# Optimization experiments

Hardware: AMD Instinct MI355X
Metric: run time of the kernel (lower is better)

## Reference

```python
import jax, jax.numpy as jnp
import numpy as np


def _retain(o1, others, W, bias):
    # o1: (b, s, h); others: (b, 4, s, h); W: (h, h); bias: (1,)
    q = o1 @ W                                        # (b, s, h)
    scores = jnp.einsum('bih,bkjh->bijk', q, others) + bias[0]  # (b, s1, s2, 4)
    w = jax.nn.softmax(scores, axis=-1)               # softmax over the 4 options
    # weight[:, :, :, k] @ option_k summed over k
    return jnp.einsum('bijk,bkjh->bih', w, others)


def setup_inputs() -> dict:
    key = jax.random.key(0)
    ks = jax.random.split(key, 7)
    b, s, h = 32, 256, 1024
    opts = {f'option{i+1}': jax.random.normal(ks[i], (b, s, h), dtype=jnp.float32)
            for i in range(5)}
    W = 0.02 * jax.random.normal(ks[5], (h, h), dtype=jnp.float32)
    bias = 0.02 * jax.random.normal(ks[6], (1,), dtype=jnp.float32)
    return {**opts, 'W': W, 'bias': bias}


def reference(option1, option2, option3, option4, option5, W, bias):
    opts = [option1, option2, option3, option4, option5]
    total = None
    for i in range(5):
        others = jnp.stack([opts[j] for j in range(5) if j != i], axis=1)  # (b,4,s,h)
        r = _retain(opts[i], others, W, bias)
        total = r if total is None else total + r
    return total / 2.0
```

## Files before the change

### kernel.cpp

```cpp
#include <hip/hip_runtime.h>
#include <hip/hip_bf16.h>
#include <stdint.h>


#define BB 32
#define SS 256
#define HH 1024

typedef __attribute__((ext_vector_type(4))) float f32x4;
typedef __attribute__((ext_vector_type(8))) __bf16 bf16x8;
typedef __attribute__((ext_vector_type(4))) __bf16 bf16x4;

__device__ constexpr int PAIR(int i, int n) { return i * 4 + (n > i ? n - 1 : n); }

__global__ void canary(float* out, float v) { out[0] = v; }

__global__ __launch_bounds__(256) void cast_all(
    const float* p0, const float* p1, const float* p2, const float* p3, const float* p4,
    __bf16* __restrict__ dst)
{
  int m = blockIdx.x >> 12;
  long off = ((long)(blockIdx.x & 4095) * 256 + threadIdx.x) * 8;
  const float* src = m == 0 ? p0 : m == 1 ? p1 : m == 2 ? p2 : m == 3 ? p3 : p4;
  float4 v0 = *(const float4*)(src + off);
  float4 v1 = *(const float4*)(src + off + 4);
  bf16x8 h;
  h[0] = (__bf16)v0.x; h[1] = (__bf16)v0.y; h[2] = (__bf16)v0.z; h[3] = (__bf16)v0.w;
  h[4] = (__bf16)v1.x; h[5] = (__bf16)v1.y; h[6] = (__bf16)v1.z; h[7] = (__bf16)v1.w;
  *(bf16x8*)(dst + (long)m * BB * SS * HH + off) = h;
}

__global__ __launch_bounds__(256) void cast_trW(const float* __restrict__ src,
                                                __bf16* __restrict__ dstT)
{
  __shared__ __bf16 tile[64][72];
  int ct = blockIdx.x & 15, rt = blockIdx.x >> 4;
  const float* s = src + (long)(rt * 64) * 1024 + ct * 64;
  int t = threadIdx.x;
#pragma unroll
  for (int p = 0; p < 4; p++) {
    int c = t + p * 256;
    int row = c >> 4, c4 = c & 15;
    float4 v = *(const float4*)(s + (long)row * 1024 + c4 * 4);
    bf16x4 h;
    h[0] = (__bf16)v.x; h[1] = (__bf16)v.y; h[2] = (__bf16)v.z; h[3] = (__bf16)v.w;
    *(bf16x4*)&tile[row][c4 * 4] = h;
  }
  __syncthreads();
#pragma unroll
  for (int p = 0; p < 4; p++) {
    int c = t + p * 256;
    int hr = c >> 4, s4 = c & 15;
    bf16x4 h;
    h[0] = tile[s4 * 4 + 0][hr];
    h[1] = tile[s4 * 4 + 1][hr];
    h[2] = tile[s4 * 4 + 2][hr];
    h[3] = tile[s4 * 4 + 3][hr];
    *(bf16x4*)(dstT + (long)(ct * 64 + hr) * 1024 + rt * 64 + s4 * 4) = h;
  }
}

__global__ __launch_bounds__(512, 2) void qgemm256(
    const __bf16* __restrict__ A, const __bf16* __restrict__ Bt, __bf16* __restrict__ C)
{
  __shared__ __align__(16) char ldsb[2 * 65536];
  int lin = blockIdx.x;
  int xcd = lin & 7, idx = lin >> 3;
  int rt = xcd * 20 + (idx >> 2), ct = idx & 3;
  int t = threadIdx.x, l = t & 63, w = t >> 6;
  int wr = w >> 2, wc = w & 3;
  f32x4 acc[8][4] = {};

  const char* gp[8];
  int wdst[8];
#pragma unroll
  for (int p = 0; p < 8; p++) {
    int c = t + 512 * (p & 3);
    int row = c >> 3, slot = c & 7;
    int wb = row * 128 + ((slot ^ (row & 7)) << 4);
    if (p < 4) {
      gp[p] = (const char*)(A + (long)(rt * 256 + row) * 1024 + slot * 8);
      wdst[p] = wb;
    } else {
      gp[p] = (const char*)(Bt + (long)(ct * 256 + row) * 1024 + slot * 8);
      wdst[p] = 32768 + wb;
    }
  }
  bf16x8 sreg[8];

#define LOADS                                                     \
  {                                                               \
    _Pragma("unroll") for (int p = 0; p < 8; p++) {               \
      sreg[p] = *(const bf16x8*)gp[p];                            \
      gp[p] += 128;                                               \
    }                                                             \
  }
#define WRITES(BUF)                                               \
  {                                                               \
    char* base = ldsb + (BUF) * 65536;                            \
    _Pragma("unroll") for (int p = 0; p < 8; p++)                 \
      *(bf16x8*)(base + wdst[p]) = sreg[p];                       \
  }

  int lr = l & 15, sl = l >> 4;
  int sx0 = (sl ^ (lr & 7)) * 16;
  int sx1 = ((4 | sl) ^ (lr & 7)) * 16;
  int arow = (wr * 128 + lr) * 128;
  int brow = 32768 + (wc * 64 + lr) * 128;

#define TILE(CUR)                                                                      \
  {                                                                                    \
    const char* base = ldsb + (CUR) * 65536;                                           \
    bf16x8 bfr[4][2], af[2][2];                                                        \
    _Pragma("unroll") for (int j = 0; j < 4; j++) {                                    \
      bfr[j][0] = *(const bf16x8*)(base + brow + j * 2048 + sx0);                      \
      bfr[j][1] = *(const bf16x8*)(base + brow + j * 2048 + sx1);                      \
    }                                                                                  \
    _Pragma("unroll") for (int ph = 0; ph < 4; ph++) {                                 \
      _Pragma("unroll") for (int ii = 0; ii < 2; ii++) {                               \
        int i = ph * 2 + ii;                                                           \
        af[ii][0] = *(const bf16x8*)(base + arow + i * 2048 + sx0);                    \
        af[ii][1] = *(const bf16x8*)(base + arow + i * 2048 + sx1);                    \
      }                                                                                \
      __builtin_amdgcn_s_setprio(1);                                                   \
      _Pragma("unroll") for (int ii = 0; ii < 2; ii++)                                 \
        _Pragma("unroll") for (int j = 0; j < 4; j++) {                                \
          acc[ph * 2 + ii][j] = __builtin_amdgcn_mfma_f32_16x16x32_bf16(               \
              af[ii][0], bfr[j][0], acc[ph * 2 + ii][j], 0, 0, 0);                     \
          acc[ph * 2 + ii][j] = __builtin_amdgcn_mfma_f32_16x16x32_bf16(               \
              af[ii][1], bfr[j][1], acc[ph * 2 + ii][j], 0, 0, 0);                     \
        }                                                                              \
      __builtin_amdgcn_s_setprio(0);                                                   \
    }                                                                                  \
  }

#define BODY(CUR, T)                                              \
  {                                                               \
    TILE(CUR)                                                     \
    if ((T) < 15) {                                               \
      asm volatile("s_waitcnt vmcnt(0)" ::: "memory");            \
      WRITES((CUR) ^ 1)                                           \
      if ((T) < 14) { LOADS }                                     \
    }                                                             \
    asm volatile("s_waitcnt lgkmcnt(0)" ::: "memory");            \
    __builtin_amdgcn_s_barrier();                                 \
  }

  LOADS
  asm volatile("s_waitcnt vmcnt(0)" ::: "memory");
  WRITES(0)
  LOADS
  asm volatile("s_waitcnt lgkmcnt(0)" ::: "memory");
  __builtin_amdgcn_s_barrier();

  for (int it = 0; it < 8; it++) {
    BODY(0, 2 * it)
    BODY(1, 2 * it + 1)
  }
#undef BODY
#undef TILE
#undef WRITES
#undef LOADS

#pragma unroll
  for (int i = 0; i < 8; i++) {
    long mrow = (long)rt * 256 + wr * 128 + i * 16 + (sl << 2);
#pragma unroll
    for (int j = 0; j < 4; j++) {
      int n = ct * 256 + wc * 64 + j * 16 + lr;
#pragma unroll
      for (int r = 0; r < 4; r++)
        C[(mrow + r) * 1024 + n] = (__bf16)acc[i][j][r];
    }
  }
}

__global__ __launch_bounds__(512, 2) void gram64(
    const __bf16* __restrict__ Q, const __bf16* __restrict__ O, __bf16* __restrict__ V)
{
  __shared__ __align__(16) char ldsb[2 * 40960];
  int bid = blockIdx.x;
  int xcd = bid & 7, idx = bid >> 3;
  int b = xcd * 4 + (idx >> 4);
  int rem = idx & 15;
  int s1t = rem >> 2, s2t = rem & 3;
  int t = threadIdx.x, l = t & 63, w = t >> 6;
  int wr = w >> 1, wc = w & 1;
  f32x4 acc[20][2] = {};

  const char* gp[5];
  int wdst[5];
#pragma unroll
  for (int p = 0; p < 5; p++) {
    int c = t + 512 * p;
    int isQ = c < 1280;
    int cc = isQ ? c : c - 1280;
    int m = cc >> 8, rr = (cc >> 2) & 63, slot = cc & 3;
    long row = (long)m * (BB * SS) + (long)b * SS + (isQ ? s1t : s2t) * 64 + rr;
    gp[p] = (const char*)((isQ ? Q : O) + row * HH + slot * 8);
    wdst[p] = (isQ ? 0 : 20480) + m * 4096 + rr * 64 + ((slot ^ ((rr >> 1) & 3)) << 4);
  }
  bf16x8 sreg[5];

#define LOADS                                                     \
  {                                                               \
    _Pragma("unroll") for (int p = 0; p < 5; p++) {               \
      sreg[p] = *(const bf16x8*)gp[p];                            \
      gp[p] += 64;                                                \
    }                                                             \
  }
#define WRITES(BUF)                                               \
  {                                                               \
    char* base = ldsb + (BUF) * 40960;                            \
    _Pragma("unroll") for (int p = 0; p < 5; p++)                 \
      *(bf16x8*)(base + wdst[p]) = sreg[p];                       \
  }

  int lr = l & 15, sl = l >> 4;
  int swz = (sl ^ ((lr >> 1) & 3)) * 16;
  int qoff = (wr * 16 + lr) * 64 + swz;
  int ooff0 = 20480 + (wc * 32 + lr) * 64 + swz;
  int ooff1 = ooff0 + 1024;

#define COMPUTE(BUF)                                                                   \
  {                                                                                    \
    const char* base = ldsb + (BUF) * 40960;                                           \
    bf16x8 qf[5], of[5];                                                               \
    _Pragma("unroll") for (int m = 0; m < 5; m++)                                      \
      qf[m] = *(const bf16x8*)(base + m * 4096 + qoff);                                \
    _Pragma("unroll") for (int m = 0; m < 5; m++)                                      \
      of[m] = *(const bf16x8*)(base + m * 4096 + ooff0);                               \
    __builtin_amdgcn_s_setprio(1);                                                     \
    _Pragma("unroll") for (int i = 0; i < 5; i++) {                                    \
      _Pragma("unroll") for (int n = 0; n < 5; n++) {                                  \
        if (n != i)                                                                    \
          acc[PAIR(i, n)][0] = __builtin_amdgcn_mfma_f32_16x16x32_bf16(                \
              qf[i], of[n], acc[PAIR(i, n)][0], 0, 0, 0);                              \
      }                                                                                \
    }                                                                                  \
    __builtin_amdgcn_s_setprio(0);                                                     \
    _Pragma("unroll") for (int m = 0; m < 5; m++)                                      \
      of[m] = *(const bf16x8*)(base + m * 4096 + ooff1);                               \
    __builtin_amdgcn_s_setprio(1);                                                     \
    _Pragma("unroll") for (int i = 0; i < 5; i++) {                                    \
      _Pragma("unroll") for (int n = 0; n < 5; n++) {                                  \
        if (n != i)                                                                    \
          acc[PAIR(i, n)][1] = __builtin_amdgcn_mfma_f32_16x16x32_bf16(                \
              qf[i], of[n], acc[PAIR(i, n)][1], 0, 0, 0);                              \
      }                                                                                \
    }                                                                                  \
    __builtin_amdgcn_s_setprio(0);                                                     \
  }

#define BODY(CUR, T)                                              \
  {                                                               \
    COMPUTE(CUR)                                                  \
    if ((T) < 31) {                                               \
      asm volatile("s_waitcnt vmcnt(0)" ::: "memory");            \
      WRITES((CUR) ^ 1)                                           \
      if ((T) < 30) { LOADS }                                     \
    }                                                             \
    asm volatile("s_waitcnt lgkmcnt(0)" ::: "memory");            \
    __builtin_amdgcn_s_barrier();                                 \
  }

  LOADS
  asm volatile("s_waitcnt vmcnt(0)" ::: "memory");
  WRITES(0)
  LOADS
  asm volatile("s_waitcnt lgkmcnt(0)" ::: "memory");
  __builtin_amdgcn_s_barrier();

  for (int it = 0; it < 16; it++) {
    BODY(0, 2 * it)
    BODY(1, 2 * it + 1)
  }
#undef BODY
#undef COMPUTE
#undef WRITES
#undef LOADS

  int s1b = s1t * 64 + wr * 16 + sl * 4;
  int s2b = s2t * 64 + wc * 32 + lr;
#pragma unroll
  for (int h = 0; h < 2; h++) {
#pragma unroll
    for (int r = 0; r < 4; r++) {
      float vacc[5] = {0.f, 0.f, 0.f, 0.f, 0.f};
#pragma unroll
      for (int i = 0; i < 5; i++) {
        float gg[5];
        float mx = -3.0e38f;
#pragma unroll
        for (int n = 0; n < 5; n++)
          if (n != i) { gg[n] = acc[PAIR(i, n)][h][r]; mx = fmaxf(mx, gg[n]); }
        float ee[5], ssum = 0.f;
#pragma unroll
        for (int n = 0; n < 5; n++)
          if (n != i) { ee[n] = __expf(gg[n] - mx); ssum += ee[n]; }
        float inv = 1.0f / ssum;
#pragma unroll
        for (int n = 0; n < 5; n++)
          if (n != i) vacc[n] += ee[n] * inv;
      }
      int s1 = s1b + r, s2 = s2b + h * 16;
#pragma unroll
      for (int n = 0; n < 5; n++)
        V[((long)(n * BB + b) * SS + s1) * SS + s2] = (__bf16)vacc[n];
    }
  }
}

__global__ __launch_bounds__(256) void pvgemm(
    const __bf16* __restrict__ Vb, const __bf16* __restrict__ Obf, float* __restrict__ out)
{
  __shared__ __bf16 smA[128][40];
  __shared__ __bf16 smB[128][40];
  int bid = blockIdx.x;
  int b = bid >> 4, s1t = (bid >> 3) & 1, ht = bid & 7;
  int t = threadIdx.x, l = t & 63, w = t >> 6;
  int wm = w >> 1, wn = w & 1;
  f32x4 acc[4][4] = {};
#pragma unroll
  for (int n = 0; n < 5; n++) {
    const __bf16* On = Obf + (long)n * BB * SS * HH;
    for (int st2 = 0; st2 < 8; st2++) {
      int s20 = st2 * 32;
#pragma unroll
      for (int p = 0; p < 2; p++) {
        int c = t + p * 256;
        int row = c >> 2, sl = c & 3;
        *(bf16x8*)&smA[row][sl * 8] =
            *(const bf16x8*)(Vb + (long)(n * BB + b) * SS * SS + (long)(s1t * 128 + row) * SS +
                             s20 + sl * 8);
      }
      {
        int h4 = (t & 31) * 4, s2q = (t >> 5) * 4;
        const __bf16* src = On + ((long)b * 256 + s20 + s2q) * 1024 + ht * 128 + h4;
        bf16x4 v0 = *(const bf16x4*)(src);
        bf16x4 v1 = *(const bf16x4*)(src + 1024);
        bf16x4 v2 = *(const bf16x4*)(src + 2048);
        bf16x4 v3 = *(const bf16x4*)(src + 3072);
        bf16x4 c0, c1, c2, c3;
        c0[0] = v0[0]; c0[1] = v1[0]; c0[2] = v2[0]; c0[3] = v3[0];
        c1[0] = v0[1]; c1[1] = v1[1]; c1[2] = v2[1]; c1[3] = v3[1];
        c2[0] = v0[2]; c2[1] = v1[2]; c2[2] = v2[2]; c2[3] = v3[2];
        c3[0] = v0[3]; c3[1] = v1[3]; c3[2] = v2[3]; c3[3] = v3[3];
        *(bf16x4*)&smB[h4 + 0][s2q] = c0;
        *(bf16x4*)&smB[h4 + 1][s2q] = c1;
        *(bf16x4*)&smB[h4 + 2][s2q] = c2;
        *(bf16x4*)&smB[h4 + 3][s2q] = c3;
      }
      __syncthreads();
      bf16x8 af[4], bfr[4];
      int sl = l >> 4, lr = l & 15;
#pragma unroll
      for (int i = 0; i < 4; i++) {
        af[i]  = *(const bf16x8*)&smA[wm * 64 + i * 16 + lr][sl * 8];
        bfr[i] = *(const bf16x8*)&smB[wn * 64 + i * 16 + lr][sl * 8];
      }
#pragma unroll
      for (int i = 0; i < 4; i++)
#pragma unroll
        for (int j = 0; j < 4; j++)
          acc[i][j] = __builtin_amdgcn_mfma_f32_16x16x32_bf16(af[i], bfr[j], acc[i][j], 0, 0, 0);
      __syncthreads();
    }
  }
#pragma unroll
  for (int i = 0; i < 4; i++) {
    int m = s1t * 128 + wm * 64 + i * 16 + ((l >> 4) << 2);
#pragma unroll
    for (int j = 0; j < 4; j++) {
      int n = ht * 128 + wn * 64 + j * 16 + (l & 15);
#pragma unroll
      for (int r = 0; r < 4; r++)
        out[(long)(b * SS + m + r) * HH + n] = 0.5f * acc[i][j][r];
    }
  }
}

extern "C" void kernel_launch(void* const* d_in, const int* in_sizes, int n_in,
                              void* d_out, int out_size, void* d_ws, size_t ws_size,
                              hipStream_t stream)
{
  const size_t SZ_W = (size_t)HH * HH * 2;
  const size_t SZ_Q = (size_t)5 * BB * SS * HH * 2;
  const size_t SZ_V = (size_t)5 * BB * SS * SS * 2;
  const size_t SZ_O = (size_t)5 * BB * SS * HH * 2;
  const size_t NEED = SZ_W + SZ_Q + SZ_V + SZ_O;
  if (ws_size < NEED) {
    canary<<<1, 1, 0, stream>>>((float*)d_out, (float)(ws_size >> 20));
    return;
  }
  char* ws = (char*)d_ws;
  __bf16* Wt  = (__bf16*)ws;
  __bf16* Qb  = (__bf16*)(ws + SZ_W);
  __bf16* Vb  = (__bf16*)(ws + SZ_W + SZ_Q);
  __bf16* Obf = (__bf16*)(ws + SZ_W + SZ_Q + SZ_V);
  const float* o0 = (const float*)d_in[0];
  const float* o1 = (const float*)d_in[1];
  const float* o2 = (const float*)d_in[2];
  const float* o3 = (const float*)d_in[3];
  const float* o4 = (const float*)d_in[4];

  cast_trW<<<256, 256, 0, stream>>>((const float*)d_in[5], Wt);
  cast_all<<<5 * 4096, 256, 0, stream>>>(o0, o1, o2, o3, o4, Obf);
  qgemm256<<<640, 512, 0, stream>>>(Obf, Wt, Qb);
  gram64<<<512, 512, 0, stream>>>(Qb, Obf, Vb);
  pvgemm<<<512, 256, 0, stream>>>(Vb, Obf, (float*)d_out);
}
```

Baseline: 274.4 us.

## Stage qgemm tiles via direct global-to-LDS loads with 4-phase pipeline

Rewrites the Q=O·W GEMM kernel's main loop to use global_load_lds (direct global-to-LDS DMA) instead of staging through registers and then writing to LDS. The K-tile is split into two halves and the M-tile into two halves, giving four phases per tile, each interleaving a staged load with MFMA work and barriers using partial vmcnt waits. This removes register pressure and VGPR-to-LDS write instructions and aims for finer-grained overlap. The trade-offs are more barriers per tile and a new LDS swizzle that must match the read pattern.

Result: no change. 269.6 us (-1.7%).

```diff
diff --git a/kernel.cpp b/kernel.cpp
--- a/kernel.cpp
+++ b/kernel.cpp
@@ -12,6 +12,11 @@
 typedef __attribute__((ext_vector_type(4))) __bf16 bf16x4;
 
 __device__ constexpr int PAIR(int i, int n) { return i * 4 + (n > i ? n - 1 : n); }
+
+__device__ __forceinline__ void gload_lds16(const void* g, void* l) {
+  __builtin_amdgcn_global_load_lds((const __attribute__((address_space(1))) void*)g,
+                                   (__attribute__((address_space(3))) void*)l, 16, 0, 0);
+}
 
 __global__ void canary(float* out, float v) { out[0] = v; }
 
@@ -69,108 +74,93 @@
   int rt = xcd * 20 + (idx >> 2), ct = idx & 3;
   int t = threadIdx.x, l = t & 63, w = t >> 6;
   int wr = w >> 2, wc = w & 3;
-  f32x4 acc[8][4] = {};
-
-  const char* gp[8];
-  int wdst[8];
-#pragma unroll
-  for (int p = 0; p < 8; p++) {
-    int c = t + 512 * (p & 3);
-    int row = c >> 3, slot = c & 7;
-    int wb = row * 128 + ((slot ^ (row & 7)) << 4);
-    if (p < 4) {
-      gp[p] = (const char*)(A + (long)(rt * 256 + row) * 1024 + slot * 8);
-      wdst[p] = wb;
-    } else {
-      gp[p] = (const char*)(Bt + (long)(ct * 256 + row) * 1024 + slot * 8);
-      wdst[p] = 32768 + wb;
+  f32x4 acc[2][4][4] = {};
+
+  const char* gp[4][2];
+  int dst[4][2];
+#pragma unroll
+  for (int h = 0; h < 4; h++) {
+#pragma unroll
+    for (int cc = 0; cc < 2; cc++) {
+      int c = t + 512 * cc;
+      int row = c >> 2;
+      int sl2 = (c & 3) ^ ((c >> 3) & 3);
+      int kh = h >> 1, isB = h & 1;
+      const __bf16* src = isB ? (Bt + (long)(ct * 256 + row) * 1024)
+                              : (A + (long)(rt * 256 + row) * 1024);
+      gp[h][cc] = (const char*)(src + kh * 32 + sl2 * 8);
+      dst[h][cc] = isB * 32768 + kh * 16384 + ((t & ~63) + 512 * cc) * 16;
     }
   }
-  bf16x8 sreg[8];
-
-#define LOADS                                                     \
-  {                                                               \
-    _Pragma("unroll") for (int p = 0; p < 8; p++) {               \
-      sreg[p] = *(const bf16x8*)gp[p];                            \
-      gp[p] += 128;                                               \
-    }                                                             \
-  }
-#define WRITES(BUF)                                               \
-  {                                                               \
-    char* base = ldsb + (BUF) * 65536;                            \
-    _Pragma("unroll") for (int p = 0; p < 8; p++)                 \
-      *(bf16x8*)(base + wdst[p]) = sreg[p];                       \
-  }
 
   int lr = l & 15, sl = l >> 4;
-  int sx0 = (sl ^ (lr & 7)) * 16;
-  int sx1 = ((4 | sl) ^ (lr & 7)) * 16;
-  int arow = (wr * 128 + lr) * 128;
-  int brow = 32768 + (wc * 64 + lr) * 128;
-
-#define TILE(CUR)                                                                      \
+  int swz = (sl ^ ((lr >> 1) & 3)) * 16;
+  int abase = (wr * 128 + lr) * 64 + swz;
+  int bbase = 32768 + (wc * 64 + lr) * 64 + swz;
+  bf16x8 bq[4];
+
+#define STAGEH(H, BUF)                                                  \
+  {                                                                     \
+    char* sb = ldsb + (BUF) * 65536;                                    \
+    gload_lds16(gp[H][0], sb + dst[H][0]);                              \
+    gload_lds16(gp[H][1], sb + dst[H][1]);                              \
+    gp[H][0] += 128; gp[H][1] += 128;                                   \
+  }
+
+#define PHASE(BUF, MH, KH, STH, DOSTAGE, VMODE)                                        \
   {                                                                                    \
-    const char* base = ldsb + (CUR) * 65536;                                           \
-    bf16x8 bfr[4][2], af[2][2];                                                        \
-    _Pragma("unroll") for (int j = 0; j < 4; j++) {                                    \
-      bfr[j][0] = *(const bf16x8*)(base + brow + j * 2048 + sx0);                      \
-      bfr[j][1] = *(const bf16x8*)(base + brow + j * 2048 + sx1);                      \
+    const char* base = ldsb + (BUF) * 65536;                                           \
+    bf16x8 af[4];                                                                      \
+    if ((MH) == 0) {                                                                   \
+      _Pragma("unroll") for (int j = 0; j < 4; j++)                                    \
+        bq[j] = *(const bf16x8*)(base + (KH) * 16384 + bbase + j * 1024);              \
     }                                                                                  \
-    _Pragma("unroll") for (int ph = 0; ph < 4; ph++) {                                 \
-      _Pragma("unroll") for (int ii = 0; ii < 2; ii++) {                               \
-        int i = ph * 2 + ii;                                                           \
-        af[ii][0] = *(const bf16x8*)(base + arow + i * 2048 + sx0);                    \
-        af[ii][1] = *(const bf16x8*)(base + arow + i * 2048 + sx1);                    \
-      }                                                                                \
-      __builtin_amdgcn_s_setprio(1);                                                   \
-      _Pragma("unroll") for (int ii = 0; ii < 2; ii++)                                 \
-        _Pragma("unroll") for (int j = 0; j < 4; j++) {                                \
-          acc[ph * 2 + ii][j] = __builtin_amdgcn_mfma_f32_16x16x32_bf16(               \
-              af[ii][0], bfr[j][0], acc[ph * 2 + ii][j], 0, 0, 0);                     \
-          acc[ph * 2 + ii][j] = __builtin_amdgcn_mfma_f32_16x16x32_bf16(               \
-              af[ii][1], bfr[j][1], acc[ph * 2 + ii][j], 0, 0, 0);                     \
-        }                                                                              \
-      __builtin_amdgcn_s_setprio(0);                                                   \
-    }                                                                                  \
-  }
-
-#define BODY(CUR, T)                                              \
-  {                                                               \
-    TILE(CUR)                                                     \
-    if ((T) < 15) {                                               \
-      asm volatile("s_waitcnt vmcnt(0)" ::: "memory");            \
-      WRITES((CUR) ^ 1)                                           \
-      if ((T) < 14) { LOADS }                                     \
-    }                                                             \
-    asm volatile("s_waitcnt lgkmcnt(0)" ::: "memory");            \
-    __builtin_amdgcn_s_barrier();                                 \
-  }
-
-  LOADS
-  asm volatile("s_waitcnt vmcnt(0)" ::: "memory");
-  WRITES(0)
-  LOADS
-  asm volatile("s_waitcnt lgkmcnt(0)" ::: "memory");
+    _Pragma("unroll") for (int i = 0; i < 4; i++)                                      \
+      af[i] = *(const bf16x8*)(base + (KH) * 16384 + abase + (MH) * 4096 + i * 1024);  \
+    if (DOSTAGE) { STAGEH(STH, (BUF) ^ 1) }                                            \
+    __builtin_amdgcn_s_barrier();                                                      \
+    asm volatile("s_waitcnt lgkmcnt(0)" ::: "memory");                                 \
+    __builtin_amdgcn_sched_barrier(0);                                                 \
+    __builtin_amdgcn_s_setprio(1);                                                     \
+    _Pragma("unroll") for (int i = 0; i < 4; i++)                                      \
+      _Pragma("unroll") for (int j = 0; j < 4; j++)                                    \
+        acc[MH][i][j] = __builtin_amdgcn_mfma_f32_16x16x32_bf16(                       \
+            af[i], bq[j], acc[MH][i][j], 0, 0, 0);                                     \
+    __builtin_amdgcn_s_setprio(0);                                                     \
+    if ((VMODE) == 4) asm volatile("s_waitcnt vmcnt(4)" ::: "memory");                 \
+    if ((VMODE) == 0) asm volatile("s_waitcnt vmcnt(0)" ::: "memory");                 \
+    __builtin_amdgcn_s_barrier();                                                      \
+  }
+
+  STAGEH(0, 0) STAGEH(1, 0) STAGEH(2, 0) STAGEH(3, 0)
+  asm volatile("s_waitcnt vmcnt(4)" ::: "memory");
   __builtin_amdgcn_s_barrier();
 
-  for (int it = 0; it < 8; it++) {
-    BODY(0, 2 * it)
-    BODY(1, 2 * it + 1)
-  }
-#undef BODY
-#undef TILE
-#undef WRITES
-#undef LOADS
-
-#pragma unroll
-  for (int i = 0; i < 8; i++) {
-    long mrow = (long)rt * 256 + wr * 128 + i * 16 + (sl << 2);
-#pragma unroll
-    for (int j = 0; j < 4; j++) {
-      int n = ct * 256 + wc * 64 + j * 16 + lr;
-#pragma unroll
-      for (int r = 0; r < 4; r++)
-        C[(mrow + r) * 1024 + n] = (__bf16)acc[i][j][r];
+  for (int tt = 0; tt < 16; tt++) {
+    int cur = tt & 1;
+    int st = tt < 15;
+    int vm1 = (tt == 15) ? 0 : 4;
+    int vm3 = (tt == 15) ? -1 : 4;
+    PHASE(cur, 0, 0, 0, st, -1)
+    PHASE(cur, 1, 0, 1, st, vm1)
+    PHASE(cur, 0, 1, 2, st, -1)
+    PHASE(cur, 1, 1, 3, st, vm3)
+  }
+#undef PHASE
+#undef STAGEH
+
+#pragma unroll
+  for (int mh = 0; mh < 2; mh++) {
+#pragma unroll
+    for (int i = 0; i < 4; i++) {
+      long mrow = (long)rt * 256 + wr * 128 + mh * 64 + i * 16 + sl * 4;
+#pragma unroll
+      for (int j = 0; j < 4; j++) {
+        int n = ct * 256 + wc * 64 + j * 16 + lr;
+#pragma unroll
+        for (int r = 0; r < 4; r++)
+          C[(mrow + r) * 1024 + n] = (__bf16)acc[mh][i][j][r];
+      }
     }
   }
 }
```

## Fuse fp32-to-bf16 cast of options into Q GEMM A-tile loading

Applied to the files above, without the earlier changes.

Removes the separate cast_all kernel. The Q GEMM now reads fp32 option tiles directly, converts them to bf16 in registers and writes them to LDS. Blocks with ct==0 also write the bf16 copy to global memory for the later kernels. The B (W transposed) tile is staged with global_load_lds straight into LDS, interleaved with the MFMA phases. This saves a full fp32 read and bf16 write round trip, but the GEMM now reads fp32 A from all four column tiles, doubling A traffic, and adds conversion work to the inner loop.

New measurement: 271.4 us. About the same (-1.1%).

```diff
diff --git a/kernel.cpp b/kernel.cpp
--- a/kernel.cpp
+++ b/kernel.cpp
@@ -13,22 +13,12 @@
 
 __device__ constexpr int PAIR(int i, int n) { return i * 4 + (n > i ? n - 1 : n); }
 
+__device__ __forceinline__ void gload_lds16(const void* g, void* l) {
+  __builtin_amdgcn_global_load_lds((const __attribute__((address_space(1))) void*)g,
+                                   (__attribute__((address_space(3))) void*)l, 16, 0, 0);
+}
+
 __global__ void canary(float* out, float v) { out[0] = v; }
-
-__global__ __launch_bounds__(256) void cast_all(
-    const float* p0, const float* p1, const float* p2, const float* p3, const float* p4,
-    __bf16* __restrict__ dst)
-{
-  int m = blockIdx.x >> 12;
-  long off = ((long)(blockIdx.x & 4095) * 256 + threadIdx.x) * 8;
-  const float* src = m == 0 ? p0 : m == 1 ? p1 : m == 2 ? p2 : m == 3 ? p3 : p4;
-  float4 v0 = *(const float4*)(src + off);
-  float4 v1 = *(const float4*)(src + off + 4);
-  bf16x8 h;
-  h[0] = (__bf16)v0.x; h[1] = (__bf16)v0.y; h[2] = (__bf16)v0.z; h[3] = (__bf16)v0.w;
-  h[4] = (__bf16)v1.x; h[5] = (__bf16)v1.y; h[6] = (__bf16)v1.z; h[7] = (__bf16)v1.w;
-  *(bf16x8*)(dst + (long)m * BB * SS * HH + off) = h;
-}
 
 __global__ __launch_bounds__(256) void cast_trW(const float* __restrict__ src,
                                                 __bf16* __restrict__ dstT)
@@ -60,46 +50,65 @@
   }
 }
 
-__global__ __launch_bounds__(512, 2) void qgemm256(
-    const __bf16* __restrict__ A, const __bf16* __restrict__ Bt, __bf16* __restrict__ C)
+__global__ __launch_bounds__(512, 2) void qgemm_f32(
+    const float* p0, const float* p1, const float* p2, const float* p3, const float* p4,
+    const __bf16* __restrict__ Bt, __bf16* __restrict__ Qb, __bf16* __restrict__ Obf)
 {
   __shared__ __align__(16) char ldsb[2 * 65536];
   int lin = blockIdx.x;
   int xcd = lin & 7, idx = lin >> 3;
   int rt = xcd * 20 + (idx >> 2), ct = idx & 3;
+  int m = rt >> 5;
+  const float* A32 = m == 0 ? p0 : m == 1 ? p1 : m == 2 ? p2 : m == 3 ? p3 : p4;
+  long arow0 = (long)(rt & 31) * 256;
   int t = threadIdx.x, l = t & 63, w = t >> 6;
   int wr = w >> 2, wc = w & 3;
   f32x4 acc[8][4] = {};
 
-  const char* gp[8];
-  int wdst[8];
-#pragma unroll
-  for (int p = 0; p < 8; p++) {
-    int c = t + 512 * (p & 3);
+  const float* ga[4];
+  __bf16* gob[4];
+  int wda[4];
+#pragma unroll
+  for (int p = 0; p < 4; p++) {
+    int c = t + 512 * p;
     int row = c >> 3, slot = c & 7;
-    int wb = row * 128 + ((slot ^ (row & 7)) << 4);
-    if (p < 4) {
-      gp[p] = (const char*)(A + (long)(rt * 256 + row) * 1024 + slot * 8);
-      wdst[p] = wb;
-    } else {
-      gp[p] = (const char*)(Bt + (long)(ct * 256 + row) * 1024 + slot * 8);
-      wdst[p] = 32768 + wb;
-    }
-  }
-  bf16x8 sreg[8];
-
-#define LOADS                                                     \
-  {                                                               \
-    _Pragma("unroll") for (int p = 0; p < 8; p++) {               \
-      sreg[p] = *(const bf16x8*)gp[p];                            \
-      gp[p] += 128;                                               \
+    ga[p] = A32 + (arow0 + row) * 1024 + slot * 8;
+    gob[p] = Obf + (long)(rt * 256 + row) * 1024 + slot * 8;
+    wda[p] = row * 128 + ((slot ^ (row & 7)) << 4);
+  }
+  const char* gb[4];
+  int wdb[4];
+#pragma unroll
+  for (int p = 0; p < 4; p++) {
+    int c = t + 512 * p;
+    int row = c >> 3;
+    int sg = (c & 7) ^ (row & 7);
+    gb[p] = (const char*)(Bt + (long)(ct * 256 + row) * 1024 + sg * 8);
+    wdb[p] = 32768 + w * 1024 + p * 8192;
+  }
+  f32x4 fa0[4], fa1[4];
+
+#define LOADS_A                                                   \
+  {                                                               \
+    _Pragma("unroll") for (int p = 0; p < 4; p++) {               \
+      fa0[p] = *(const f32x4*)ga[p];                              \
+      fa1[p] = *(const f32x4*)(ga[p] + 4);                        \
+      ga[p] += 64;                                                \
     }                                                             \
   }
-#define WRITES(BUF)                                               \
+#define CVTWR(BUF)                                                \
   {                                                               \
     char* base = ldsb + (BUF) * 65536;                            \
-    _Pragma("unroll") for (int p = 0; p < 8; p++)                 \
-      *(bf16x8*)(base + wdst[p]) = sreg[p];                       \
+    _Pragma("unroll") for (int p = 0; p < 4; p++) {               \
+      bf16x8 h;                                                   \
+      h[0] = (__bf16)fa0[p][0]; h[1] = (__bf16)fa0[p][1];         \
+      h[2] = (__bf16)fa0[p][2]; h[3] = (__bf16)fa0[p][3];         \
+      h[4] = (__bf16)fa1[p][0]; h[5] = (__bf16)fa1[p][1];         \
+      h[6] = (__bf16)fa1[p][2]; h[7] = (__bf16)fa1[p][3];         \
+      *(bf16x8*)(base + wda[p]) = h;                              \
+      if (ct == 0) *(bf16x8*)gob[p] = h;                          \
+      gob[p] += 64;                                               \
+    }                                                             \
   }
 
   int lr = l & 15, sl = l >> 4;
@@ -108,15 +117,20 @@
   int arow = (wr * 128 + lr) * 128;
   int brow = 32768 + (wc * 64 + lr) * 128;
 
-#define TILE(CUR)                                                                      \
+#define TILE(CUR, DOSTAGE)                                                             \
   {                                                                                    \
     const char* base = ldsb + (CUR) * 65536;                                           \
+    char* sbase = ldsb + ((CUR) ^ 1) * 65536;                                          \
     bf16x8 bfr[4][2], af[2][2];                                                        \
     _Pragma("unroll") for (int j = 0; j < 4; j++) {                                    \
       bfr[j][0] = *(const bf16x8*)(base + brow + j * 2048 + sx0);                      \
       bfr[j][1] = *(const bf16x8*)(base + brow + j * 2048 + sx1);                      \
     }                                                                                  \
     _Pragma("unroll") for (int ph = 0; ph < 4; ph++) {                                 \
+      if (DOSTAGE) {                                                                   \
+        gload_lds16(gb[ph], sbase + wdb[ph]);                                          \
+        gb[ph] += 128;                                                                 \
+      }                                                                                \
       _Pragma("unroll") for (int ii = 0; ii < 2; ii++) {                               \
         int i = ph * 2 + ii;                                                           \
         af[ii][0] = *(const bf16x8*)(base + arow + i * 2048 + sx0);                    \
@@ -136,41 +150,46 @@
 
 #define BODY(CUR, T)                                              \
   {                                                               \
-    TILE(CUR)                                                     \
+    TILE(CUR, (T) < 15)                                           \
     if ((T) < 15) {                                               \
       asm volatile("s_waitcnt vmcnt(0)" ::: "memory");            \
-      WRITES((CUR) ^ 1)                                           \
-      if ((T) < 14) { LOADS }                                     \
+      CVTWR((CUR) ^ 1)                                            \
+      if ((T) < 14) { LOADS_A }                                   \
     }                                                             \
     asm volatile("s_waitcnt lgkmcnt(0)" ::: "memory");            \
     __builtin_amdgcn_s_barrier();                                 \
   }
 
-  LOADS
+  LOADS_A
+#pragma unroll
+  for (int p = 0; p < 4; p++) {
+    gload_lds16(gb[p], ldsb + wdb[p]);
+    gb[p] += 128;
+  }
   asm volatile("s_waitcnt vmcnt(0)" ::: "memory");
-  WRITES(0)
-  LOADS
+  CVTWR(0)
+  LOADS_A
   asm volatile("s_waitcnt lgkmcnt(0)" ::: "memory");
   __builtin_amdgcn_s_barrier();
 
-  for (int it = 0; it < 8; it++) {
-    BODY(0, 2 * it)
-    BODY(1, 2 * it + 1)
-  }
+  for (int tt = 0; tt < 15; tt++) {
+    BODY(tt & 1, tt)
+  }
+  TILE(1, 0)
 #undef BODY
 #undef TILE
-#undef WRITES
-#undef LOADS
+#undef CVTWR
+#undef LOADS_A
 
 #pragma unroll
   for (int i = 0; i < 8; i++) {
-    long mrow = (long)rt * 256 + wr * 128 + i * 16 + (sl << 2);
+    long mrow = (long)rt * 256 + wr * 128 + i * 16 + sl * 4;
 #pragma unroll
     for (int j = 0; j < 4; j++) {
       int n = ct * 256 + wc * 64 + j * 16 + lr;
 #pragma unroll
       for (int r = 0; r < 4; r++)
-        C[(mrow + r) * 1024 + n] = (__bf16)acc[i][j][r];
+        Qb[(mrow + r) * 1024 + n] = (__bf16)acc[i][j][r];
     }
   }
 }
@@ -405,8 +424,7 @@
   const float* o4 = (const float*)d_in[4];
 
   cast_trW<<<256, 256, 0, stream>>>((const float*)d_in[5], Wt);
-  cast_all<<<5 * 4096, 256, 0, stream>>>(o0, o1, o2, o3, o4, Obf);
-  qgemm256<<<640, 512, 0, stream>>>(Obf, Wt, Qb);
+  qgemm_f32<<<640, 512, 0, stream>>>(o0, o1, o2, o3, o4, Wt, Qb, Obf);
   gram64<<<512, 512, 0, stream>>>(Qb, Obf, Vb);
   pvgemm<<<512, 256, 0, stream>>>(Vb, Obf, (float*)d_out);
 }
```

## Rewrite Q GEMM with 128-row tiles and direct global-to-LDS async loads

Applied to the files above, without the earlier changes.

The Q projection GEMM now uses 128x256 tiles instead of 256x256 and launches 1280 blocks instead of 640. Global loads go straight into LDS via global_load_lds, spread across the MFMA phases. This replaces the register-staged load/write pipeline, which is meant to cut VGPR pressure and overlap copies with compute. The trade-offs are a smaller per-wave accumulator (less reuse of the B tile), launch bounds of 1 block per CU given the 96KB of LDS, and an XOR swizzle that is now applied on the global-address side.

New measurement: 270.3 us. Within noise of the previous version (-1.5%).

```diff
diff --git a/kernel.cpp b/kernel.cpp
--- a/kernel.cpp
+++ b/kernel.cpp
@@ -12,6 +12,11 @@
 typedef __attribute__((ext_vector_type(4))) __bf16 bf16x4;
 
 __device__ constexpr int PAIR(int i, int n) { return i * 4 + (n > i ? n - 1 : n); }
+
+__device__ __forceinline__ void gload_lds16(const void* g, void* l) {
+  __builtin_amdgcn_global_load_lds((const __attribute__((address_space(1))) void*)g,
+                                   (__attribute__((address_space(3))) void*)l, 16, 0, 0);
+}
 
 __global__ void canary(float* out, float v) { out[0] = v; }
 
@@ -60,111 +65,99 @@
   }
 }
 
-__global__ __launch_bounds__(512, 2) void qgemm256(
+__global__ __launch_bounds__(512, 1) void qgemm128(
     const __bf16* __restrict__ A, const __bf16* __restrict__ Bt, __bf16* __restrict__ C)
 {
-  __shared__ __align__(16) char ldsb[2 * 65536];
+  __shared__ __align__(16) char ldsb[2 * 49152];
   int lin = blockIdx.x;
   int xcd = lin & 7, idx = lin >> 3;
-  int rt = xcd * 20 + (idx >> 2), ct = idx & 3;
+  int rt = xcd * 40 + (idx >> 2), ct = idx & 3;
   int t = threadIdx.x, l = t & 63, w = t >> 6;
   int wr = w >> 2, wc = w & 3;
-  f32x4 acc[8][4] = {};
-
-  const char* gp[8];
-  int wdst[8];
-#pragma unroll
-  for (int p = 0; p < 8; p++) {
-    int c = t + 512 * (p & 3);
-    int row = c >> 3, slot = c & 7;
-    int wb = row * 128 + ((slot ^ (row & 7)) << 4);
-    if (p < 4) {
-      gp[p] = (const char*)(A + (long)(rt * 256 + row) * 1024 + slot * 8);
-      wdst[p] = wb;
-    } else {
-      gp[p] = (const char*)(Bt + (long)(ct * 256 + row) * 1024 + slot * 8);
-      wdst[p] = 32768 + wb;
-    }
-  }
-  bf16x8 sreg[8];
-
-#define LOADS                                                     \
-  {                                                               \
-    _Pragma("unroll") for (int p = 0; p < 8; p++) {               \
-      sreg[p] = *(const bf16x8*)gp[p];                            \
-      gp[p] += 128;                                               \
-    }                                                             \
-  }
-#define WRITES(BUF)                                               \
-  {                                                               \
-    char* base = ldsb + (BUF) * 65536;                            \
-    _Pragma("unroll") for (int p = 0; p < 8; p++)                 \
-      *(bf16x8*)(base + wdst[p]) = sreg[p];                       \
+  f32x4 acc[4][4] = {};
+
+  const char* gA[2];
+  int dA[2];
+#pragma unroll
+  for (int p = 0; p < 2; p++) {
+    int c = t + 512 * p;
+    int row = c >> 3;
+    int sg = (c & 7) ^ (row & 7);
+    gA[p] = (const char*)(A + (long)(rt * 128 + row) * 1024 + sg * 8);
+    dA[p] = ((t & ~63) + 512 * p) * 16;
+  }
+  const char* gB[4];
+  int dB[4];
+#pragma unroll
+  for (int p = 0; p < 4; p++) {
+    int c = t + 512 * p;
+    int row = c >> 3;
+    int sg = (c & 7) ^ (row & 7);
+    gB[p] = (const char*)(Bt + (long)(ct * 256 + row) * 1024 + sg * 8);
+    dB[p] = 16384 + ((t & ~63) + 512 * p) * 16;
   }
 
   int lr = l & 15, sl = l >> 4;
   int sx0 = (sl ^ (lr & 7)) * 16;
   int sx1 = ((4 | sl) ^ (lr & 7)) * 16;
-  int arow = (wr * 128 + lr) * 128;
-  int brow = 32768 + (wc * 64 + lr) * 128;
-
-#define TILE(CUR)                                                                      \
+  int arow = (wr * 64 + lr) * 128;
+  int brow = 16384 + (wc * 64 + lr) * 128;
+
+#define TILE(CUR, DOSTAGE)                                                             \
   {                                                                                    \
-    const char* base = ldsb + (CUR) * 65536;                                           \
-    bf16x8 bfr[4][2], af[2][2];                                                        \
+    const char* base = ldsb + (CUR) * 49152;                                           \
+    char* sbase = ldsb + ((CUR) ^ 1) * 49152;                                          \
+    bf16x8 bfr[4][2], af[2];                                                           \
     _Pragma("unroll") for (int j = 0; j < 4; j++) {                                    \
       bfr[j][0] = *(const bf16x8*)(base + brow + j * 2048 + sx0);                      \
       bfr[j][1] = *(const bf16x8*)(base + brow + j * 2048 + sx1);                      \
     }                                                                                  \
     _Pragma("unroll") for (int ph = 0; ph < 4; ph++) {                                 \
-      _Pragma("unroll") for (int ii = 0; ii < 2; ii++) {                               \
-        int i = ph * 2 + ii;                                                           \
-        af[ii][0] = *(const bf16x8*)(base + arow + i * 2048 + sx0);                    \
-        af[ii][1] = *(const bf16x8*)(base + arow + i * 2048 + sx1);                    \
+      if (DOSTAGE) {                                                                   \
+        if (ph == 0) {                                                                 \
+          gload_lds16(gA[0], sbase + dA[0]); gA[0] += 128;                             \
+          gload_lds16(gA[1], sbase + dA[1]); gA[1] += 128;                             \
+        } else if (ph == 1) {                                                          \
+          gload_lds16(gB[0], sbase + dB[0]); gB[0] += 128;                             \
+          gload_lds16(gB[1], sbase + dB[1]); gB[1] += 128;                             \
+        } else if (ph == 2) {                                                          \
+          gload_lds16(gB[2], sbase + dB[2]); gB[2] += 128;                             \
+        } else {                                                                       \
+          gload_lds16(gB[3], sbase + dB[3]); gB[3] += 128;                             \
+        }                                                                              \
       }                                                                                \
+      af[0] = *(const bf16x8*)(base + arow + ph * 2048 + sx0);                         \
+      af[1] = *(const bf16x8*)(base + arow + ph * 2048 + sx1);                         \
       __builtin_amdgcn_s_setprio(1);                                                   \
-      _Pragma("unroll") for (int ii = 0; ii < 2; ii++)                                 \
-        _Pragma("unroll") for (int j = 0; j < 4; j++) {                                \
-          acc[ph * 2 + ii][j] = __builtin_amdgcn_mfma_f32_16x16x32_bf16(               \
-              af[ii][0], bfr[j][0], acc[ph * 2 + ii][j], 0, 0, 0);                     \
-          acc[ph * 2 + ii][j] = __builtin_amdgcn_mfma_f32_16x16x32_bf16(               \
-              af[ii][1], bfr[j][1], acc[ph * 2 + ii][j], 0, 0, 0);                     \
-        }                                                                              \
+      _Pragma("unroll") for (int j = 0; j < 4; j++) {                                  \
+        acc[ph][j] = __builtin_amdgcn_mfma_f32_16x16x32_bf16(                          \
+            af[0], bfr[j][0], acc[ph][j], 0, 0, 0);                                    \
+        acc[ph][j] = __builtin_amdgcn_mfma_f32_16x16x32_bf16(                          \
+            af[1], bfr[j][1], acc[ph][j], 0, 0, 0);                                    \
+      }                                                                                \
       __builtin_amdgcn_s_setprio(0);                                                   \
     }                                                                                  \
   }
 
-#define BODY(CUR, T)                                              \
-  {                                                               \
-    TILE(CUR)                                                     \
-    if ((T) < 15) {                                               \
-      asm volatile("s_waitcnt vmcnt(0)" ::: "memory");            \
-      WRITES((CUR) ^ 1)                                           \
-      if ((T) < 14) { LOADS }                                     \
-    }                                                             \
-    asm volatile("s_waitcnt lgkmcnt(0)" ::: "memory");            \
-    __builtin_amdgcn_s_barrier();                                 \
-  }
-
-  LOADS
+  {
+#pragma unroll
+    for (int p = 0; p < 2; p++) { gload_lds16(gA[p], ldsb + dA[p]); gA[p] += 128; }
+#pragma unroll
+    for (int p = 0; p < 4; p++) { gload_lds16(gB[p], ldsb + dB[p]); gB[p] += 128; }
+  }
   asm volatile("s_waitcnt vmcnt(0)" ::: "memory");
-  WRITES(0)
-  LOADS
-  asm volatile("s_waitcnt lgkmcnt(0)" ::: "memory");
   __builtin_amdgcn_s_barrier();
-
-  for (int it = 0; it < 8; it++) {
-    BODY(0, 2 * it)
-    BODY(1, 2 * it + 1)
-  }
-#undef BODY
+  for (int tt = 0; tt < 15; tt++) {
+    TILE(tt & 1, 1)
+    asm volatile("s_waitcnt vmcnt(0)" ::: "memory");
+    __builtin_amdgcn_s_barrier();
+  }
+  TILE(1, 0)
 #undef TILE
-#undef WRITES
-#undef LOADS
-
-#pragma unroll
-  for (int i = 0; i < 8; i++) {
-    long mrow = (long)rt * 256 + wr * 128 + i * 16 + (sl << 2);
+
+#pragma unroll
+  for (int i = 0; i < 4; i++) {
+    long mrow = (long)rt * 128 + wr * 64 + i * 16 + sl * 4;
 #pragma unroll
     for (int j = 0; j < 4; j++) {
       int n = ct * 256 + wc * 64 + j * 16 + lr;
@@ -406,7 +399,7 @@
 
   cast_trW<<<256, 256, 0, stream>>>((const float*)d_in[5], Wt);
   cast_all<<<5 * 4096, 256, 0, stream>>>(o0, o1, o2, o3, o4, Obf);
-  qgemm256<<<640, 512, 0, stream>>>(Obf, Wt, Qb);
+  qgemm128<<<1280, 512, 0, stream>>>(Obf, Wt, Qb);
   gram64<<<512, 512, 0, stream>>>(Qb, Obf, Vb);
   pvgemm<<<512, 256, 0, stream>>>(Vb, Obf, (float*)d_out);
 }
```
